# Performance work log

Measured on AMD Instinct MI355X. Metric: run time of the kernel, lower is better.

The kernel has to match this reference:

```python
import jax, jax.numpy as jnp
import numpy as np

HIDDEN = 4096
NUM_HEADS = 32
NUM_KV_HEADS = 8
HEAD_DIM = 128
T = 2048
ROPE_THETA = 10000.0


def setup_inputs() -> dict:
    key = jax.random.key(0)
    ks = jax.random.split(key, 10)
    s = 0.02
    return {
        "hidden_states": jax.random.normal(ks[0], (T, HIDDEN), dtype=jnp.float32),
        "positions": jnp.arange(T, dtype=jnp.int32),
        "Wq": jax.random.normal(ks[1], (NUM_HEADS * HEAD_DIM, HIDDEN), dtype=jnp.float32) * s,
        "bq": jax.random.normal(ks[2], (NUM_HEADS * HEAD_DIM,), dtype=jnp.float32) * s,
        "Wk": jax.random.normal(ks[3], (NUM_KV_HEADS * HEAD_DIM, HIDDEN), dtype=jnp.float32) * s,
        "bk": jax.random.normal(ks[4], (NUM_KV_HEADS * HEAD_DIM,), dtype=jnp.float32) * s,
        "Wv": jax.random.normal(ks[5], (NUM_KV_HEADS * HEAD_DIM, HIDDEN), dtype=jnp.float32) * s,
        "bv": jax.random.normal(ks[6], (NUM_KV_HEADS * HEAD_DIM,), dtype=jnp.float32) * s,
        "Wo": jax.random.normal(ks[7], (HIDDEN, HIDDEN), dtype=jnp.float32) * s,
        "bo": jax.random.normal(ks[8], (HIDDEN,), dtype=jnp.float32) * s,
    }


def _rope_cos_sin(positions, head_dim, base):
    # neox-style rotary over the full head_dim
    half = head_dim // 2
    inv_freq = 1.0 / (base ** (jnp.arange(0, half, dtype=jnp.float32) * 2.0 / head_dim))
    angles = positions.astype(jnp.float32)[:, None] * inv_freq[None, :]  # [T, half]
    return jnp.cos(angles), jnp.sin(angles)


def _apply_rope(x, cos, sin):
    # x: [T, H, D]; neox: split halves, rotate
    half = x.shape[-1] // 2
    x1, x2 = x[..., :half], x[..., half:]
    c = cos[:, None, :]
    s = sin[:, None, :]
    return jnp.concatenate([x1 * c - x2 * s, x2 * c + x1 * s], axis=-1)


def reference(hidden_states, positions, Wq, bq, Wk, bk, Wv, bv, Wo, bo):
    q = (hidden_states @ Wq.T + bq).reshape(T, NUM_HEADS, HEAD_DIM)
    k = (hidden_states @ Wk.T + bk).reshape(T, NUM_KV_HEADS, HEAD_DIM)
    v = (hidden_states @ Wv.T + bv).reshape(T, NUM_KV_HEADS, HEAD_DIM)

    cos, sin = _rope_cos_sin(positions, HEAD_DIM, ROPE_THETA)
    q = _apply_rope(q, cos, sin)
    k = _apply_rope(k, cos, sin)

    scale = 1.0 / np.sqrt(HEAD_DIM).astype(np.float32)
    group = NUM_HEADS // NUM_KV_HEADS
    qg = q.reshape(T, NUM_KV_HEADS, group, HEAD_DIM)
    # scores: [g_kv, r, q, k] without materializing repeated KV heads
    scores = jnp.einsum('qgrd,kgd->grqk', qg, k) * scale
    causal = positions[:, None] >= positions[None, :]  # [T, T]
    scores = jnp.where(causal[None, None], scores, jnp.finfo(scores.dtype).min)
    probs = jax.nn.softmax(scores, axis=-1)
    o = jnp.einsum('grqk,kgd->qgrd', probs, v).reshape(T, NUM_HEADS * HEAD_DIM)
    return o @ Wo.T + bo
```

## Files before the change

kernel.cpp:

```cpp
#include <hip/hip_runtime.h>
#include <stdint.h>

typedef unsigned short u16;
typedef __bf16 bf16x8_t __attribute__((ext_vector_type(8)));
typedef float f32x4_t __attribute__((ext_vector_type(4)));

#define T_SEQ 2048
#define HID 4096
#define ROWQKV 6144

__device__ __forceinline__ float bf2f(u16 x){ return __uint_as_float(((uint32_t)x)<<16); }
__device__ __forceinline__ u16 f2bf(float f){
  uint32_t u = __float_as_uint(f);
  return (u16)((u + 0x7fffu + ((u>>16)&1u)) >> 16);
}

__device__ __forceinline__ void gload16(const void* g, void* l){
  __builtin_amdgcn_global_load_lds(
      (const __attribute__((address_space(1))) uint32_t*)g,
      (__attribute__((address_space(3))) uint32_t*)l, 16, 0, 0);
}

__global__ void cvt_kernel(const float* __restrict__ src, u16* __restrict__ dst, int n8){
  int i = blockIdx.x*blockDim.x + threadIdx.x;
  if (i >= n8) return;
  const float4* s = (const float4*)src;
  float4 a = s[2*i], b = s[2*i+1];
  union { u16 u[8]; uint4 v; } o;
  o.u[0]=f2bf(a.x); o.u[1]=f2bf(a.y); o.u[2]=f2bf(a.z); o.u[3]=f2bf(a.w);
  o.u[4]=f2bf(b.x); o.u[5]=f2bf(b.y); o.u[6]=f2bf(b.z); o.u[7]=f2bf(b.w);
  ((uint4*)dst)[i] = o.v;
}

__global__ void setup_kernel(const float* __restrict__ bq, const float* __restrict__ bk,
                             const float* __restrict__ bv, const int* __restrict__ pos,
                             float* __restrict__ bqkv, float* __restrict__ cost,
                             float* __restrict__ sint){
  int i = blockIdx.x*blockDim.x + threadIdx.x;
  if (i < 6144) bqkv[i] = (i<4096) ? bq[i] : ((i<5120) ? bk[i-4096] : bv[i-5120]);
  if (i < T_SEQ*64){
    int t = i >> 6, d = i & 63;
    float inv = powf(10000.0f, -(float)(2*d) / 128.0f);
    float ang = (float)pos[t] * inv;
    cost[i] = cosf(ang);
    sint[i] = sinf(ang);
  }
}

#define GBAR __builtin_amdgcn_s_barrier()
#define LGKM0 do{ asm volatile("s_waitcnt lgkmcnt(0)" ::: "memory"); \
                  __builtin_amdgcn_sched_barrier(0); }while(0)

#define BUF6 28672

#define AREAD6(mh, ck) do{ \
  const u16* ab = &lds[cur + aoff + (mh)*4096]; \
  afr[0] = *(const bf16x8_t*)&ab[0*1024 + (ck)]; \
  afr[1] = *(const bf16x8_t*)&ab[1*1024 + (ck)]; \
  afr[2] = *(const bf16x8_t*)&ab[2*1024 + (ck)]; \
  afr[3] = *(const bf16x8_t*)&ab[3*1024 + (ck)]; }while(0)

#define BREAD6(ck) do{ \
  const u16* bb = &lds[cur + boff]; \
  bfr[0] = *(const bf16x8_t*)&bb[0*1024 + (ck)]; \
  bfr[1] = *(const bf16x8_t*)&bb[1*1024 + (ck)]; \
  bfr[2] = *(const bf16x8_t*)&bb[2*1024 + (ck)]; }while(0)

#define MM12(mh) do{ \
  _Pragma("unroll") \
  for (int mi=0; mi<4; ++mi){ \
    _Pragma("unroll") \
    for (int n=0; n<3; ++n) \
      acc[(mh)*4+mi][n] = __builtin_amdgcn_mfma_f32_16x16x32_bf16(afr[mi], bfr[n], acc[(mh)*4+mi][n],0,0,0); \
  } }while(0)

__global__ __launch_bounds__(512, 2)
void gemm_qkv(const u16* __restrict__ A, const u16* __restrict__ B,
              const float* __restrict__ bias, u16* __restrict__ Cb,
              int K, int N)
{
  __shared__ u16 lds[2*BUF6];
  const int tid = threadIdx.x, lane = tid & 63, w = tid >> 6;
  const int l15 = lane & 15, l4 = lane >> 4;
  const int wm = w >> 2, wn = w & 3;

  const int nwg = gridDim.x * gridDim.y;
  int flat = blockIdx.y * gridDim.x + blockIdx.x;
  flat = (flat & 7) * (nwg >> 3) + (flat >> 3);
  const int bx = flat % gridDim.x, by = flat / gridDim.x;
  const int bm = by * 256, bn = bx * 192;

  const int srow = w*8 + (lane >> 3);
  const int swc  = ((lane & 7) ^ (lane >> 3)) * 8;
  const u16* pA = A + (size_t)(bm + srow)*K + swc;
  const u16* pB = B + (size_t)(bn + srow)*K + swc;
  const size_t j64 = (size_t)64*K;
  const int wu = w*512;

  const int cA0 = ((0 + l4) ^ (l15 & 7)) * 8;
  const int cA1 = ((4 + l4) ^ (l15 & 7)) * 8;
  const int aoff = (wm*128 + l15) * 64;
  const int boff = 16384 + (wn*48 + l15) * 64;

  f32x4_t acc[8][3] = {};
  const int KT = K >> 6;

  gload16(pA + 0*j64, &lds[0     + wu]);
  gload16(pA + 1*j64, &lds[4096  + wu]);
  gload16(pA + 2*j64, &lds[8192  + wu]);
  gload16(pA + 3*j64, &lds[12288 + wu]);
  gload16(pB + 0*j64, &lds[16384 + wu]);
  gload16(pB + 1*j64, &lds[20480 + wu]);
  gload16(pB + 2*j64, &lds[24576 + wu]);
  pA += 64; pB += 64;
  asm volatile("s_waitcnt vmcnt(0)" ::: "memory");
  GBAR;

  for (int t = 0; t < KT; ++t){
    const int cur = (t & 1) * BUF6;
    const int nxt = ((t + 1) & 1) * BUF6;
    const bool st = (t + 1 < KT);
    bf16x8_t afr[4], bfr[3];

    BREAD6(cA0); AREAD6(0, cA0);
    if (st){
      gload16(pA + 0*j64, &lds[nxt + 0     + wu]);
      gload16(pA + 1*j64, &lds[nxt + 4096  + wu]);
      gload16(pA + 2*j64, &lds[nxt + 8192  + wu]);
      gload16(pA + 3*j64, &lds[nxt + 12288 + wu]);
    }
    GBAR; LGKM0;
    __builtin_amdgcn_s_setprio(1); MM12(0); __builtin_amdgcn_s_setprio(0);
    GBAR;

    AREAD6(1, cA0);
    if (st){
      gload16(pB + 0*j64, &lds[nxt + 16384 + wu]);
      gload16(pB + 1*j64, &lds[nxt + 20480 + wu]);
      gload16(pB + 2*j64, &lds[nxt + 24576 + wu]);
      pA += 64; pB += 64;
    }
    GBAR; LGKM0;
    __builtin_amdgcn_s_setprio(1); MM12(1); __builtin_amdgcn_s_setprio(0);
    GBAR;

    BREAD6(cA1); AREAD6(0, cA1);
    GBAR; LGKM0;
    __builtin_amdgcn_s_setprio(1); MM12(0); __builtin_amdgcn_s_setprio(0);
    GBAR;

    AREAD6(1, cA1);
    GBAR; LGKM0;
    __builtin_amdgcn_s_setprio(1); MM12(1); __builtin_amdgcn_s_setprio(0);
    if (st) asm volatile("s_waitcnt vmcnt(0)" ::: "memory");
    GBAR;
  }

  #pragma unroll
  for (int m=0;m<8;m++){
    #pragma unroll
    for (int n=0;n<3;n++){
      #pragma unroll
      for (int j=0;j<4;j++){
        int row = bm + wm*128 + (m>>2)*64 + (m&3)*16 + l4*4 + j;
        int col = bn + wn*48 + n*16 + l15;
        Cb[(size_t)row*N + col] = f2bf(acc[m][n][j] + bias[col]);
      }
    }
  }
}

#define BUFK 24576

#define KMREAD(ck) do{ \
  afr[0] = *(const bf16x8_t*)&lds[cur + aoff + 0*1024 + (ck)]; \
  afr[1] = *(const bf16x8_t*)&lds[cur + aoff + 1*1024 + (ck)]; \
  afr[2] = *(const bf16x8_t*)&lds[cur + aoff + 2*1024 + (ck)]; \
  afr[3] = *(const bf16x8_t*)&lds[cur + aoff + 3*1024 + (ck)]; \
  bfr[0] = *(const bf16x8_t*)&lds[cur + boff + 0*1024 + (ck)]; \
  bfr[1] = *(const bf16x8_t*)&lds[cur + boff + 1*1024 + (ck)]; \
  bfr[2] = *(const bf16x8_t*)&lds[cur + boff + 2*1024 + (ck)]; \
  bfr[3] = *(const bf16x8_t*)&lds[cur + boff + 3*1024 + (ck)]; }while(0)

#define MM16KM do{ \
  _Pragma("unroll") \
  for (int mi=0; mi<4; ++mi){ \
    _Pragma("unroll") \
    for (int n=0; n<4; ++n) \
      acc[mi][n] = __builtin_amdgcn_mfma_f32_16x16x32_bf16(afr[mi], bfr[n], acc[mi][n],0,0,0); \
  } }while(0)

__global__ __launch_bounds__(512, 2)
void gemm_km(const u16* __restrict__ A, const u16* __restrict__ B,
             const float* __restrict__ bias, float* __restrict__ Cf,
             int K, int N)
{
  __shared__ u16 lds[3*BUFK];
  const int tid = threadIdx.x, lane = tid & 63, w = tid >> 6;
  const int l15 = lane & 15, l4 = lane >> 4;
  const int wm = w >> 1, wn = w & 1;

  const int nwg = gridDim.x * gridDim.y;
  int flat = blockIdx.y * gridDim.x + blockIdx.x;
  flat = (flat & 7) * (nwg >> 3) + (flat >> 3);
  const int bx = flat % gridDim.x, by = flat / gridDim.x;
  const int bm = by * 256, bn = bx * 128;

  const int srow = w*8 + (lane >> 3);
  const int swc  = ((lane & 7) ^ (lane >> 3)) * 8;
  const u16* pA = A + (size_t)(bm + srow)*K + swc;
  const u16* pB = B + (size_t)(bn + srow)*K + swc;
  const size_t j64 = (size_t)64*K;
  const int wu = w*512;

  const int cA0 = ((0 + l4) ^ (l15 & 7)) * 8;
  const int cA1 = ((4 + l4) ^ (l15 & 7)) * 8;
  const int aoff = (wm*64 + l15) * 64;
  const int boff = 16384 + (wn*64 + l15) * 64;

  f32x4_t acc[4][4] = {};
  const int KT = K >> 6;

  gload16(pA + 0*j64,      &lds[0*4096 + wu]);
  gload16(pA + 1*j64,      &lds[1*4096 + wu]);
  gload16(pA + 2*j64,      &lds[2*4096 + wu]);
  gload16(pA + 3*j64,      &lds[3*4096 + wu]);
  gload16(pB + 0*j64,      &lds[16384 + 0*4096 + wu]);
  gload16(pB + 1*j64,      &lds[16384 + 1*4096 + wu]);
  gload16(pA + 64 + 0*j64, &lds[BUFK + 0*4096 + wu]);
  gload16(pA + 64 + 1*j64, &lds[BUFK + 1*4096 + wu]);
  gload16(pA + 64 + 2*j64, &lds[BUFK + 2*4096 + wu]);
  gload16(pA + 64 + 3*j64, &lds[BUFK + 3*4096 + wu]);
  gload16(pB + 64 + 0*j64, &lds[BUFK + 16384 + 0*4096 + wu]);
  gload16(pB + 64 + 1*j64, &lds[BUFK + 16384 + 1*4096 + wu]);
  pA += 128; pB += 128;
  asm volatile("s_waitcnt vmcnt(6)" ::: "memory");
  GBAR;

  for (int t = 0; t < KT; ++t){
    const int cur = (t % 3) * BUFK;
    const int sb  = ((t + 2) % 3) * BUFK;
    const bool st = (t + 2 < KT);
    bf16x8_t afr[4], bfr[4];

    KMREAD(cA0);
    if (st){
      gload16(pA + 0*j64, &lds[sb + 0*4096 + wu]);
      gload16(pA + 1*j64, &lds[sb + 1*4096 + wu]);
      gload16(pA + 2*j64, &lds[sb + 2*4096 + wu]);
    }
    GBAR; LGKM0;
    __builtin_amdgcn_s_setprio(1); MM16KM; __builtin_amdgcn_s_setprio(0);
    GBAR;

    KMREAD(cA1);
    if (st){
      gload16(pA + 3*j64, &lds[sb + 3*4096 + wu]);
      gload16(pB + 0*j64, &lds[sb + 16384 + 0*4096 + wu]);
      gload16(pB + 1*j64, &lds[sb + 16384 + 1*4096 + wu]);
      pA += 64; pB += 64;
    }
    GBAR; LGKM0;
    __builtin_amdgcn_s_setprio(1); MM16KM; __builtin_amdgcn_s_setprio(0);
    if (st)              asm volatile("s_waitcnt vmcnt(6)" ::: "memory");
    else if (t + 1 < KT) asm volatile("s_waitcnt vmcnt(0)" ::: "memory");
    GBAR;
  }

  #pragma unroll
  for (int mi=0;mi<4;mi++){
    #pragma unroll
    for (int n=0;n<4;n++){
      #pragma unroll
      for (int j=0;j<4;j++){
        int row = bm + wm*64 + mi*16 + l4*4 + j;
        int col = bn + wn*64 + n*16 + l15;
        Cf[(size_t)row*N + col] = acc[mi][n][j] + bias[col];
      }
    }
  }
}

__global__ void rope_kernel(u16* __restrict__ qkv, const float* __restrict__ cost,
                            const float* __restrict__ sint){
  int i = blockIdx.x*blockDim.x + threadIdx.x;
  int t = i / 2560;
  int r = i % 2560;
  int h = r >> 6, d = r & 63;
  int base = (h < 32) ? h*128 : (4096 + (h-32)*128);
  size_t p1 = (size_t)t*ROWQKV + base + d;
  float x1 = bf2f(qkv[p1]), x2 = bf2f(qkv[p1+64]);
  float c = cost[(t<<6)+d], s = sint[(t<<6)+d];
  qkv[p1]    = f2bf(x1*c - x2*s);
  qkv[p1+64] = f2bf(x2*c + x1*s);
}

#define VOFF 16384
#define POFF 24576

__global__ __launch_bounds__(256)
void attn_kernel(const u16* __restrict__ qkv, u16* __restrict__ attn_o)
{
  __shared__ u16 lds[28672];
  const int tid = threadIdx.x, lane = tid&63, wid = tid>>6;
  const int l15 = lane&15, l4 = lane>>4;
  const int l7 = l15 & 7;
  const int h  = blockIdx.x & 31;
  const int qt = 31 - (blockIdx.x >> 5);
  const int q0 = qt * 64;
  const int kvh = h >> 2;
  const u16* Qg = qkv + h*128;
  const u16* Kg = qkv + 4096 + kvh*128;
  const u16* Vg = qkv + 5120 + kvh*128;

  bf16x8_t qf[4];
  {
    size_t qrow = (size_t)(q0 + wid*16 + l15);
    #pragma unroll
    for (int kk=0;kk<4;kk++)
      qf[kk] = *(const bf16x8_t*)(Qg + qrow*ROWQKV + kk*32 + l4*8);
  }
  float mrow[4] = {-1e30f,-1e30f,-1e30f,-1e30f};
  float lrow[4] = {0.f,0.f,0.f,0.f};
  f32x4_t oacc[8] = {};
  const float scale = 0.08838834764831845f;

  const u16* ksrc[4];
  int kls[4];
  #pragma unroll
  for (int i=0;i<4;i++){
    const int c = wid*4 + i;
    ksrc[i] = Kg + (size_t)((c&7)*8 + (lane>>3))*ROWQKV
               + (c>>3)*64 + ((lane&7)^(lane>>3))*8;
    kls[i] = c*512;
  }
  const int kvp = tid & 31;
  const int vd0 = (tid >> 5) * 16;
  uint4 rv[4];

  #pragma unroll
  for (int i=0;i<4;i++) gload16(ksrc[i], &lds[kls[i]]);
  #pragma unroll
  for (int i=0;i<4;i++) ksrc[i] += (size_t)64*ROWQKV;
  {
    const u16* va = Vg + (size_t)(2*kvp)*ROWQKV + vd0;
    rv[0] = *(const uint4*)va;            rv[1] = *(const uint4*)(va + 8);
    rv[2] = *(const uint4*)(va + ROWQKV); rv[3] = *(const uint4*)(va + ROWQKV + 8);
  }
  __syncthreads();
  {
    const u16* ra = (const u16*)&rv[0]; const u16* rb = (const u16*)&rv[2];
    #pragma unroll
    for (int e=0;e<8;e++)
      *(uint32_t*)&lds[VOFF + (vd0+e)*64 + ((kvp>>2)^(e&7))*8 + 2*(kvp&3)]
          = (uint32_t)ra[e] | ((uint32_t)rb[e] << 16);
    ra = (const u16*)&rv[1]; rb = (const u16*)&rv[3];
    #pragma unroll
    for (int e=0;e<8;e++)
      *(uint32_t*)&lds[VOFF + (vd0+8+e)*64 + ((kvp>>2)^(e&7))*8 + 2*(kvp&3)]
          = (uint32_t)ra[e] | ((uint32_t)rb[e] << 16);
  }
  __syncthreads();

  for (int kt = 0; kt <= qt; ++kt){
    const int kv0 = kt * 64;
    const int kcur = (kt & 1) * 8192;
    const bool pre = (kt < qt);
    if (pre){
      const int knxt = ((kt+1) & 1) * 8192;
      #pragma unroll
      for (int i=0;i<4;i++) gload16(ksrc[i], &lds[knxt + kls[i]]);
      #pragma unroll
      for (int i=0;i<4;i++) ksrc[i] += (size_t)64*ROWQKV;
      const u16* va = Vg + (size_t)(kv0 + 64 + 2*kvp)*ROWQKV + vd0;
      rv[0] = *(const uint4*)va;            rv[1] = *(const uint4*)(va + 8);
      rv[2] = *(const uint4*)(va + ROWQKV); rv[3] = *(const uint4*)(va + ROWQKV + 8);
    }

    f32x4_t sacc[4] = {};
    #pragma unroll
    for (int n=0;n<4;n++){
      #pragma unroll
      for (int kk=0;kk<4;kk++){
        bf16x8_t kf = *(const bf16x8_t*)&lds[kcur + (kk>>1)*4096
                        + (n*16+l15)*64 + (((kk&1)*4 + l4) ^ l7)*8];
        sacc[n] = __builtin_amdgcn_mfma_f32_16x16x32_bf16(qf[kk], kf, sacc[n], 0,0,0);
      }
    }
    float sv[4][4];
    float pmax[4] = {-1e30f,-1e30f,-1e30f,-1e30f};
    bool diag = (kt == qt);
    #pragma unroll
    for (int n=0;n<4;n++){
      int kvcol = kv0 + n*16 + l15;
      #pragma unroll
      for (int j=0;j<4;j++){
        float s = sacc[n][j] * scale;
        int qrow = q0 + wid*16 + l4*4 + j;
        if (diag && kvcol > qrow) s = -1e30f;
        sv[n][j] = s;
        pmax[j] = fmaxf(pmax[j], s);
      }
    }
    #pragma unroll
    for (int off=1; off<16; off<<=1){
      #pragma unroll
      for (int j=0;j<4;j++)
        pmax[j] = fmaxf(pmax[j], __shfl_xor(pmax[j], off, 64));
    }
    float esc[4], rsum[4] = {0.f,0.f,0.f,0.f};
    #pragma unroll
    for (int j=0;j<4;j++){
      float mn = fmaxf(mrow[j], pmax[j]);
      esc[j] = __expf(mrow[j] - mn);
      mrow[j] = mn;
    }
    #pragma unroll
    for (int n=0;n<4;n++){
      #pragma unroll
      for (int j=0;j<4;j++){
        float p = __expf(sv[n][j] - mrow[j]);
        sv[n][j] = p;
        rsum[j] += p;
      }
    }
    #pragma unroll
    for (int off=1; off<16; off<<=1){
      #pragma unroll
      for (int j=0;j<4;j++)
        rsum[j] += __shfl_xor(rsum[j], off, 64);
    }
    #pragma unroll
    for (int j=0;j<4;j++) lrow[j] = lrow[j]*esc[j] + rsum[j];
    #pragma unroll
    for (int n=0;n<8;n++){
      #pragma unroll
      for (int j=0;j<4;j++) oacc[n][j] *= esc[j];
    }
    #pragma unroll
    for (int n=0;n<4;n++){
      #pragma unroll
      for (int j=0;j<4;j++)
        lds[POFF + (wid*16 + l4*4 + j)*64
            + (((n*2 + (l15>>3)) ^ ((l4*4+j)&7))*8) + l7] = f2bf(sv[n][j]);
    }
    #pragma unroll
    for (int kk=0;kk<2;kk++){
      const int blk = ((kk*4 + l4) ^ l7)*8;
      bf16x8_t pf = *(const bf16x8_t*)&lds[POFF + (wid*16 + l15)*64 + blk];
      #pragma unroll
      for (int n=0;n<8;n++){
        bf16x8_t vf = *(const bf16x8_t*)&lds[VOFF + (n*16 + l15)*64 + blk];
        oacc[n] = __builtin_amdgcn_mfma_f32_16x16x32_bf16(pf, vf, oacc[n], 0,0,0);
      }
    }
    __syncthreads();
    if (pre){
      const u16* ra = (const u16*)&rv[0]; const u16* rb = (const u16*)&rv[2];
      #pragma unroll
      for (int e=0;e<8;e++)
        *(uint32_t*)&lds[VOFF + (vd0+e)*64 + ((kvp>>2)^(e&7))*8 + 2*(kvp&3)]
            = (uint32_t)ra[e] | ((uint32_t)rb[e] << 16);
      ra = (const u16*)&rv[1]; rb = (const u16*)&rv[3];
      #pragma unroll
      for (int e=0;e<8;e++)
        *(uint32_t*)&lds[VOFF + (vd0+8+e)*64 + ((kvp>>2)^(e&7))*8 + 2*(kvp&3)]
            = (uint32_t)ra[e] | ((uint32_t)rb[e] << 16);
    }
    __syncthreads();
  }

  #pragma unroll
  for (int n=0;n<8;n++){
    #pragma unroll
    for (int j=0;j<4;j++){
      int qrow = q0 + wid*16 + l4*4 + j;
      int col  = h*128 + n*16 + l15;
      attn_o[(size_t)qrow*HID + col] = f2bf(oacc[n][j] / lrow[j]);
    }
  }
}

extern "C" void kernel_launch(void* const* d_in, const int* in_sizes, int n_in,
                              void* d_out, int out_size, void* d_ws, size_t ws_size,
                              hipStream_t stream)
{
  const float* hs = (const float*)d_in[0];
  const int*  pos = (const int*)d_in[1];
  const float* Wq = (const float*)d_in[2];
  const float* bq = (const float*)d_in[3];
  const float* Wk = (const float*)d_in[4];
  const float* bk = (const float*)d_in[5];
  const float* Wv = (const float*)d_in[6];
  const float* bv = (const float*)d_in[7];
  const float* Wo = (const float*)d_in[8];
  const float* bo = (const float*)d_in[9];
  float* out = (float*)d_out;

  char* ws = (char*)d_ws;
  u16* hs_bf   = (u16*)ws;  ws += (size_t)2048*4096*2;
  u16* Wqkv_bf = (u16*)ws;  ws += (size_t)6144*4096*2;
  u16* Wo_bf   = (u16*)ws;  ws += (size_t)4096*4096*2;
  u16* qkv     = (u16*)ws;  ws += (size_t)2048*6144*2;
  u16* attn_b  = (u16*)ws;  ws += (size_t)2048*4096*2;
  float* bqkv  = (float*)ws; ws += (size_t)6144*4;
  float* cost  = (float*)ws; ws += (size_t)2048*64*4;
  float* sint  = (float*)ws; ws += (size_t)2048*64*4;

  {
    int n8 = 2048*4096/8;
    cvt_kernel<<<(n8+255)/256, 256, 0, stream>>>(hs, hs_bf, n8);
    n8 = 4096*4096/8;
    cvt_kernel<<<(n8+255)/256, 256, 0, stream>>>(Wq, Wqkv_bf, n8);
    n8 = 1024*4096/8;
    cvt_kernel<<<(n8+255)/256, 256, 0, stream>>>(Wk, Wqkv_bf + (size_t)4096*4096, n8);
    cvt_kernel<<<(n8+255)/256, 256, 0, stream>>>(Wv, Wqkv_bf + (size_t)5120*4096, n8);
    n8 = 4096*4096/8;
    cvt_kernel<<<(n8+255)/256, 256, 0, stream>>>(Wo, Wo_bf, n8);
  }
  setup_kernel<<<(T_SEQ*64 + 255)/256, 256, 0, stream>>>(bq, bk, bv, pos, bqkv, cost, sint);

  gemm_qkv<<<dim3(6144/192, 2048/256), 512, 0, stream>>>(hs_bf, Wqkv_bf, bqkv, qkv, 4096, 6144);
  rope_kernel<<<(T_SEQ*40*64)/256, 256, 0, stream>>>(qkv, cost, sint);
  attn_kernel<<<1024, 256, 0, stream>>>(qkv, attn_b);
  gemm_km<<<dim3(4096/128, 2048/256), 512, 0, stream>>>(attn_b, Wo_bf, bo, out, 4096, 4096);
}
```

Before: 341.5 us.

## Fold softmax row-sum into MFMA via ones column, lazy rescale, exp2

The attention kernel now computes the softmax denominator by appending a 16-row block of bf16 ones to the V tile in LDS, so a ninth MFMA accumulator gathers the row sums. This removes the per-tile shuffle reduction for the row sums. It also folds the scale into a log2e-based exp2 and rescales the running max only when some row's new max exceeds the stored max by more than 8 in log2 units, checked wave-wide. Probabilities are packed with v_cvt_pk_bf16_f32. In exchange each tile issues extra MFMAs, needs more LDS, and sums bf16-rounded probabilities, which slightly changes accuracy.

```diff
diff --git a/kernel.cpp b/kernel.cpp
--- a/kernel.cpp
+++ b/kernel.cpp
@@ -19,6 +19,12 @@
   __builtin_amdgcn_global_load_lds(
       (const __attribute__((address_space(1))) uint32_t*)g,
       (__attribute__((address_space(3))) uint32_t*)l, 16, 0, 0);
+}
+
+__device__ __forceinline__ uint32_t cvtpk(float lo, float hi_){
+  uint32_t r;
+  asm("v_cvt_pk_bf16_f32 %0, %1, %2" : "=v"(r) : "v"(lo), "v"(hi_));
+  return r;
 }
 
 __global__ void cvt_kernel(const float* __restrict__ src, u16* __restrict__ dst, int n8){
@@ -296,12 +302,12 @@
 }
 
 #define VOFF 16384
-#define POFF 24576
+#define POFF 25600
 
 __global__ __launch_bounds__(256)
 void attn_kernel(const u16* __restrict__ qkv, u16* __restrict__ attn_o)
 {
-  __shared__ u16 lds[28672];
+  __shared__ u16 lds[29696];
   const int tid = threadIdx.x, lane = tid&63, wid = tid>>6;
   const int l15 = lane&15, l4 = lane>>4;
   const int l7 = l15 & 7;
@@ -312,6 +318,7 @@
   const u16* Qg = qkv + h*128;
   const u16* Kg = qkv + 4096 + kvh*128;
   const u16* Vg = qkv + 5120 + kvh*128;
+  const float c2 = 0.127543147f;
 
   bf16x8_t qf[4];
   {
@@ -320,10 +327,8 @@
     for (int kk=0;kk<4;kk++)
       qf[kk] = *(const bf16x8_t*)(Qg + qrow*ROWQKV + kk*32 + l4*8);
   }
-  float mrow[4] = {-1e30f,-1e30f,-1e30f,-1e30f};
-  float lrow[4] = {0.f,0.f,0.f,0.f};
-  f32x4_t oacc[8] = {};
-  const float scale = 0.08838834764831845f;
+  float M[4] = {-1e30f,-1e30f,-1e30f,-1e30f};
+  f32x4_t oacc[9] = {};
 
   const u16* ksrc[4];
   int kls[4];
@@ -346,6 +351,8 @@
     const u16* va = Vg + (size_t)(2*kvp)*ROWQKV + vd0;
     rv[0] = *(const uint4*)va;            rv[1] = *(const uint4*)(va + 8);
     rv[2] = *(const uint4*)(va + ROWQKV); rv[3] = *(const uint4*)(va + ROWQKV + 8);
+    *(uint32_t*)&lds[VOFF + 8192 + tid*4]     = 0x3F803F80u;
+    *(uint32_t*)&lds[VOFF + 8192 + tid*4 + 2] = 0x3F803F80u;
   }
   __syncthreads();
   {
@@ -395,7 +402,7 @@
       int kvcol = kv0 + n*16 + l15;
       #pragma unroll
       for (int j=0;j<4;j++){
-        float s = sacc[n][j] * scale;
+        float s = sacc[n][j];
         int qrow = q0 + wid*16 + l4*4 + j;
         if (diag && kvcol > qrow) s = -1e30f;
         sv[n][j] = s;
@@ -408,48 +415,52 @@
       for (int j=0;j<4;j++)
         pmax[j] = fmaxf(pmax[j], __shfl_xor(pmax[j], off, 64));
     }
-    float esc[4], rsum[4] = {0.f,0.f,0.f,0.f};
-    #pragma unroll
-    for (int j=0;j<4;j++){
-      float mn = fmaxf(mrow[j], pmax[j]);
-      esc[j] = __expf(mrow[j] - mn);
-      mrow[j] = mn;
+    {
+      float pm2[4];
+      #pragma unroll
+      for (int j=0;j<4;j++) pm2[j] = pmax[j] * c2;
+      bool near = (pm2[0]-M[0] <= 8.0f) && (pm2[1]-M[1] <= 8.0f)
+               && (pm2[2]-M[2] <= 8.0f) && (pm2[3]-M[3] <= 8.0f);
+      if (!__all(near)){
+        float es[4];
+        #pragma unroll
+        for (int j=0;j<4;j++){
+          float mn = fmaxf(M[j], pm2[j]);
+          es[j] = exp2f(M[j] - mn);
+          M[j] = mn;
+        }
+        #pragma unroll
+        for (int n=0;n<9;n++){
+          #pragma unroll
+          for (int j=0;j<4;j++) oacc[n][j] *= es[j];
+        }
+      }
     }
     #pragma unroll
     for (int n=0;n<4;n++){
       #pragma unroll
-      for (int j=0;j<4;j++){
-        float p = __expf(sv[n][j] - mrow[j]);
-        sv[n][j] = p;
-        rsum[j] += p;
-      }
-    }
-    #pragma unroll
-    for (int off=1; off<16; off<<=1){
-      #pragma unroll
       for (int j=0;j<4;j++)
-        rsum[j] += __shfl_xor(rsum[j], off, 64);
-    }
-    #pragma unroll
-    for (int j=0;j<4;j++) lrow[j] = lrow[j]*esc[j] + rsum[j];
-    #pragma unroll
-    for (int n=0;n<8;n++){
-      #pragma unroll
-      for (int j=0;j<4;j++) oacc[n][j] *= esc[j];
-    }
-    #pragma unroll
-    for (int n=0;n<4;n++){
-      #pragma unroll
-      for (int j=0;j<4;j++)
-        lds[POFF + (wid*16 + l4*4 + j)*64
-            + (((n*2 + (l15>>3)) ^ ((l4*4+j)&7))*8) + l7] = f2bf(sv[n][j]);
+        sv[n][j] = exp2f(fmaf(sv[n][j], c2, -M[j]));
+    }
+    {
+      const int r0 = wid*16 + l4*4;
+      #pragma unroll
+      for (int n=0;n<4;n++){
+        uint32_t p01 = cvtpk(sv[n][0], sv[n][1]);
+        uint32_t p23 = cvtpk(sv[n][2], sv[n][3]);
+        const int cb = n*2 + (l15>>3);
+        lds[POFF + (r0+0)*64 + ((cb ^ ((r0+0)&7))*8) + l7] = (u16)p01;
+        lds[POFF + (r0+1)*64 + ((cb ^ ((r0+1)&7))*8) + l7] = (u16)(p01 >> 16);
+        lds[POFF + (r0+2)*64 + ((cb ^ ((r0+2)&7))*8) + l7] = (u16)p23;
+        lds[POFF + (r0+3)*64 + ((cb ^ ((r0+3)&7))*8) + l7] = (u16)(p23 >> 16);
+      }
     }
     #pragma unroll
     for (int kk=0;kk<2;kk++){
       const int blk = ((kk*4 + l4) ^ l7)*8;
       bf16x8_t pf = *(const bf16x8_t*)&lds[POFF + (wid*16 + l15)*64 + blk];
       #pragma unroll
-      for (int n=0;n<8;n++){
+      for (int n=0;n<9;n++){
         bf16x8_t vf = *(const bf16x8_t*)&lds[VOFF + (n*16 + l15)*64 + blk];
         oacc[n] = __builtin_amdgcn_mfma_f32_16x16x32_bf16(pf, vf, oacc[n], 0,0,0);
       }
@@ -470,13 +481,18 @@
     __syncthreads();
   }
 
-  #pragma unroll
-  for (int n=0;n<8;n++){
-    #pragma unroll
-    for (int j=0;j<4;j++){
-      int qrow = q0 + wid*16 + l4*4 + j;
-      int col  = h*128 + n*16 + l15;
-      attn_o[(size_t)qrow*HID + col] = f2bf(oacc[n][j] / lrow[j]);
+  {
+    float inv[4];
+    #pragma unroll
+    for (int j=0;j<4;j++) inv[j] = 1.0f / oacc[8][j];
+    #pragma unroll
+    for (int n=0;n<8;n++){
+      #pragma unroll
+      for (int j=0;j<4;j++){
+        int qrow = q0 + wid*16 + l4*4 + j;
+        int col  = h*128 + n*16 + l15;
+        attn_o[(size_t)qrow*HID + col] = f2bf(oacc[n][j] * inv[j]);
+      }
     }
   }
 }
```

Result: slower. 432.9 us (+26.8%).
